# Kernel optimization log

Measured on AMD Instinct MI355X. Metric: run time of the kernel, lower is better.

## Reference

```python
import jax, jax.numpy as jnp
import numpy as np

N_NODES = 50000
IN_CH = 256
HID_CH = 64
N_EDGES = 800000


def setup_inputs() -> dict:
    key = jax.random.key(0)
    k1, k2, k3, k4, k5 = jax.random.split(key, 5)
    x = jax.random.normal(k1, (N_NODES, IN_CH), dtype=jnp.float32)
    edge_index = jax.random.randint(k2, (2, N_EDGES), 0, N_NODES, dtype=jnp.int64)
    # GCNConv linear weight (Glorot) and zero bias, as in PyG defaults
    W = jax.random.normal(k3, (IN_CH, HID_CH), dtype=jnp.float32) * (1.0 / np.sqrt(IN_CH))
    bias = jnp.zeros((HID_CH,), dtype=jnp.float32)
    # PReLU per-channel weight, torch default init 0.25
    prelu_a = jnp.full((HID_CH,), 0.25, dtype=jnp.float32)
    return {"x": x, "edge_index": edge_index, "W": W, "bias": bias, "prelu_a": prelu_a}


def reference(x, edge_index, W, bias, prelu_a):
    # GCNConv, normalize=False: transform then scatter-add over edges, + bias
    xw = x @ W                               # [N, H]
    src, dst = edge_index[0], edge_index[1]
    msgs = xw[src]                           # [E, H] gather
    agg = jax.ops.segment_sum(msgs, dst, num_segments=N_NODES)  # [N, H]
    out = agg + bias
    # per-channel PReLU
    return jnp.where(out > 0, out, prelu_a * out)
```

## Files before the change

kernel.cpp:

```cpp
#include <hip/hip_runtime.h>

#define N_NODES 50000
#define IN_CH   256
#define HID_CH  64
#define N_EDGES 800000

#define NBUCKET 391
#define AG_ROWS 128
#define PTILE   4096
#define CAP     4096

typedef __attribute__((ext_vector_type(8))) short short8;
typedef __attribute__((ext_vector_type(4))) float f32x4;

static __device__ __forceinline__ unsigned short f2bf(float f) {
    unsigned int u = __float_as_uint(f);
    u += 0x7FFF + ((u >> 16) & 1);
    return (unsigned short)(u >> 16);
}
static __device__ __forceinline__ float bf2f(unsigned short h) {
    return __uint_as_float(((unsigned int)h) << 16);
}

__global__ __launch_bounds__(256) void wfrag_kernel(const float* __restrict__ W,
                                                    unsigned short* __restrict__ wfrag) {
    const int idx = blockIdx.x * 256 + threadIdx.x;
    if (idx >= 2048) return;
    const int ks = idx >> 8;
    const int nt = (idx >> 6) & 3;
    const int l  = idx & 63;
    const int q = l >> 4, m = l & 15;
    const int n = nt * 16 + m;
    const int k0 = ks * 32 + q * 8;
    short8 v;
    #pragma unroll
    for (int j = 0; j < 8; ++j) v[j] = (short)f2bf(W[(k0 + j) * HID_CH + n]);
    ((short8*)wfrag)[idx] = v;
}

__global__ __launch_bounds__(256) void gemm_kernel(const float* __restrict__ x,
                                                   const unsigned short* __restrict__ wfrag,
                                                   unsigned short* __restrict__ xwb) {
    const int wave = threadIdx.x >> 6;
    const int lane = threadIdx.x & 63;
    const int q = lane >> 4, m = lane & 15;
    const int row0 = blockIdx.x * 64 + wave * 16;
    const int arow = row0 + m;
    const int arl = arow < N_NODES ? arow : N_NODES - 1;
    const float* xr = x + (size_t)arl * IN_CH + q * 8;
    const short8* wf = (const short8*)wfrag;

    f32x4 acc0 = {0.f,0.f,0.f,0.f}, acc1 = acc0, acc2 = acc0, acc3 = acc0;

    #pragma unroll
    for (int ks = 0; ks < 8; ++ks) {
        const float4 a0 = *(const float4*)(xr + ks * 32);
        const float4 a1 = *(const float4*)(xr + ks * 32 + 4);
        short8 af;
        af[0] = (short)f2bf(a0.x); af[1] = (short)f2bf(a0.y);
        af[2] = (short)f2bf(a0.z); af[3] = (short)f2bf(a0.w);
        af[4] = (short)f2bf(a1.x); af[5] = (short)f2bf(a1.y);
        af[6] = (short)f2bf(a1.z); af[7] = (short)f2bf(a1.w);
        const short8 b0 = wf[(ks * 4 + 0) * 64 + lane];
        const short8 b1 = wf[(ks * 4 + 1) * 64 + lane];
        const short8 b2 = wf[(ks * 4 + 2) * 64 + lane];
        const short8 b3 = wf[(ks * 4 + 3) * 64 + lane];
        acc0 = __builtin_amdgcn_mfma_f32_16x16x32_bf16(af, b0, acc0, 0, 0, 0);
        acc1 = __builtin_amdgcn_mfma_f32_16x16x32_bf16(af, b1, acc1, 0, 0, 0);
        acc2 = __builtin_amdgcn_mfma_f32_16x16x32_bf16(af, b2, acc2, 0, 0, 0);
        acc3 = __builtin_amdgcn_mfma_f32_16x16x32_bf16(af, b3, acc3, 0, 0, 0);
    }

    #pragma unroll
    for (int r = 0; r < 4; ++r) {
        const int row = row0 + q * 4 + r;
        if (row < N_NODES) {
            unsigned short* o = xwb + (size_t)row * HID_CH + m;
            o[0]  = f2bf(acc0[r]);
            o[16] = f2bf(acc1[r]);
            o[32] = f2bf(acc2[r]);
            o[48] = f2bf(acc3[r]);
        }
    }
}

__global__ __launch_bounds__(256) void bhist_kernel(const int* __restrict__ ei,
                                                    int* __restrict__ cnt) {
    __shared__ int h[NBUCKET];
    for (int i = threadIdx.x; i < NBUCKET; i += 256) h[i] = 0;
    __syncthreads();
    for (int e = blockIdx.x * 256 + threadIdx.x; e < N_EDGES; e += gridDim.x * 256)
        atomicAdd(&h[ei[N_EDGES + e] >> 7], 1);
    __syncthreads();
    for (int i = threadIdx.x; i < NBUCKET; i += 256)
        if (h[i]) atomicAdd(&cnt[i], h[i]);
}

__global__ __launch_bounds__(512) void bscan_kernel(int* __restrict__ cur,
                                                    int* __restrict__ bucket_off) {
    __shared__ int s[512];
    const int t = threadIdx.x;
    const int v = (t < NBUCKET) ? cur[t] : 0;
    s[t] = v;
    __syncthreads();
    for (int off = 1; off < 512; off <<= 1) {
        const int a = s[t];
        const int add = (t >= off) ? s[t - off] : 0;
        __syncthreads();
        s[t] = a + add;
        __syncthreads();
    }
    const int ex = s[t] - v;
    if (t < NBUCKET) { bucket_off[t] = ex; cur[t] = ex; }
    if (t == 0) bucket_off[NBUCKET] = N_EDGES;
}

__global__ __launch_bounds__(512) void partition_kernel(const int* __restrict__ ei,
                                                        int* __restrict__ cur,
                                                        unsigned int* __restrict__ packed_out) {
    __shared__ int cnt[512];
    __shared__ int excl[512];
    __shared__ int lcur[512];
    __shared__ int gbase[512];
    __shared__ unsigned int staged[PTILE];
    __shared__ unsigned short sbkt[PTILE];

    const int t = threadIdx.x;
    const int tile0 = blockIdx.x * PTILE;
    const int tcnt = min(PTILE, N_EDGES - tile0);

    cnt[t] = 0;
    __syncthreads();

    int es[8], ed[8];
    #pragma unroll
    for (int i = 0; i < 8; ++i) {
        const int e = tile0 + t + i * 512;
        if (e < N_EDGES) {
            es[i] = ei[e];
            ed[i] = ei[N_EDGES + e];
            atomicAdd(&cnt[ed[i] >> 7], 1);
        } else es[i] = -1;
    }
    __syncthreads();

    const int v = cnt[t];
    excl[t] = v;
    __syncthreads();
    for (int off = 1; off < 512; off <<= 1) {
        const int a = excl[t];
        const int add = (t >= off) ? excl[t - off] : 0;
        __syncthreads();
        excl[t] = a + add;
        __syncthreads();
    }
    const int ex = excl[t] - v;
    __syncthreads();
    excl[t] = ex;
    lcur[t] = ex;
    if (t < NBUCKET && v > 0) gbase[t] = atomicAdd(&cur[t], v);
    __syncthreads();

    #pragma unroll
    for (int i = 0; i < 8; ++i) {
        if (es[i] >= 0) {
            const int b = ed[i] >> 7;
            const int pos = atomicAdd(&lcur[b], 1);
            staged[pos] = ((unsigned int)(ed[i] & 127) << 16) | (unsigned int)es[i];
            sbkt[pos] = (unsigned short)b;
        }
    }
    __syncthreads();

    #pragma unroll
    for (int i = 0; i < 8; ++i) {
        const int idx = t + i * 512;
        if (idx < tcnt) {
            const int b = sbkt[idx];
            packed_out[gbase[b] + (idx - excl[b])] = staged[idx];
        }
    }
}

__global__ __launch_bounds__(1024) void aggregate_kernel(const unsigned short* __restrict__ xwb,
                                                         const unsigned int* __restrict__ packed,
                                                         const int* __restrict__ bucket_off,
                                                         const float* __restrict__ bias,
                                                         const float* __restrict__ prelu_a,
                                                         float* __restrict__ out) {
    __shared__ unsigned int   sp[CAP];
    __shared__ unsigned short ssrc[CAP];
    __shared__ int hcnt[AG_ROWS];
    __shared__ int hexcl[AG_ROWS];
    __shared__ int hcur[AG_ROWS];
    __shared__ float acc[AG_ROWS * HID_CH];

    const int b = blockIdx.x;
    const int t = threadIdx.x;
    const int beg = bucket_off[b], end = bucket_off[b + 1];
    const int wv = t >> 6, lane = t & 63;
    const int slot = lane >> 4, c0 = (lane & 15) * 4;

    #pragma unroll
    for (int i = 0; i < 8; ++i) acc[t + i * 1024] = 0.f;

    for (int cbeg = beg; cbeg < end; cbeg += CAP) {
        const int csz = min(CAP, end - cbeg);

        if (t < AG_ROWS) hcnt[t] = 0;
        __syncthreads();

        for (int i = t; i < csz; i += 1024) {
            const unsigned int p = packed[cbeg + i];
            sp[i] = p;
            atomicAdd(&hcnt[p >> 16], 1);
        }
        __syncthreads();

        if (t < AG_ROWS) hexcl[t] = hcnt[t];
        __syncthreads();
        for (int off = 1; off < AG_ROWS; off <<= 1) {
            int nv = 0;
            if (t < AG_ROWS) { nv = hexcl[t]; if (t >= off) nv += hexcl[t - off]; }
            __syncthreads();
            if (t < AG_ROWS) hexcl[t] = nv;
            __syncthreads();
        }
        if (t < AG_ROWS) { const int e = hexcl[t] - hcnt[t]; hexcl[t] = e; hcur[t] = e; }
        __syncthreads();

        for (int i = t; i < csz; i += 1024) {
            const unsigned int p = sp[i];
            const int pos = atomicAdd(&hcur[p >> 16], 1);
            ssrc[pos] = (unsigned short)(p & 0xFFFFu);
        }
        __syncthreads();

        #pragma unroll
        for (int k = 0; k < 8; ++k) {
            const int nl = wv + k * 16;
            const int rb = hexcl[nl];
            const int re = rb + hcnt[nl];
            float4 a4 = make_float4(0.f, 0.f, 0.f, 0.f);
            for (int i = rb + slot; i < re; i += 4) {
                const int s = ssrc[i];
                const ushort4 v = *(const ushort4*)(xwb + (size_t)s * HID_CH + c0);
                a4.x += bf2f(v.x); a4.y += bf2f(v.y);
                a4.z += bf2f(v.z); a4.w += bf2f(v.w);
            }
            a4.x += __shfl_xor(a4.x, 16, 64); a4.y += __shfl_xor(a4.y, 16, 64);
            a4.z += __shfl_xor(a4.z, 16, 64); a4.w += __shfl_xor(a4.w, 16, 64);
            a4.x += __shfl_xor(a4.x, 32, 64); a4.y += __shfl_xor(a4.y, 32, 64);
            a4.z += __shfl_xor(a4.z, 32, 64); a4.w += __shfl_xor(a4.w, 32, 64);
            if (slot == 0) {
                float4* ap = (float4*)&acc[nl * HID_CH + c0];
                float4 c4 = *ap;
                c4.x += a4.x; c4.y += a4.y; c4.z += a4.z; c4.w += a4.w;
                *ap = c4;
            }
        }
        __syncthreads();
    }

    const int node0 = b * AG_ROWS;
    const int nrows = min(AG_ROWS, N_NODES - node0);
    for (int i = t; i < nrows * (HID_CH / 4); i += 1024) {
        const int r = i >> 4;
        const int cc = (i & 15) * 4;
        const float4 a4 = *(float4*)&acc[r * HID_CH + cc];
        const float4 bb = *(const float4*)(bias + cc);
        const float4 aa = *(const float4*)(prelu_a + cc);
        float4 rr;
        rr.x = a4.x + bb.x; rr.x = rr.x > 0.f ? rr.x : aa.x * rr.x;
        rr.y = a4.y + bb.y; rr.y = rr.y > 0.f ? rr.y : aa.y * rr.y;
        rr.z = a4.z + bb.z; rr.z = rr.z > 0.f ? rr.z : aa.z * rr.z;
        rr.w = a4.w + bb.w; rr.w = rr.w > 0.f ? rr.w : aa.w * rr.w;
        *(float4*)(out + (size_t)(node0 + r) * HID_CH + cc) = rr;
    }
}

extern "C" void kernel_launch(void* const* d_in, const int* in_sizes, int n_in,
                              void* d_out, int out_size, void* d_ws, size_t ws_size,
                              hipStream_t stream) {
    const float* x       = (const float*)d_in[0];
    const int*   ei      = (const int*)d_in[1];
    const float* W       = (const float*)d_in[2];
    const float* bias    = (const float*)d_in[3];
    const float* prelu_a = (const float*)d_in[4];
    float* out = (float*)d_out;

    char* w = (char*)d_ws;
    unsigned short* xwb        = (unsigned short*)(w);
    int*            cur        = (int*)(w + 6400000);
    int*            bucket_off = (int*)(w + 6401600);
    unsigned int*   packed     = (unsigned int*)(w + 6403200);
    unsigned short* wfrag      = (unsigned short*)(w + 9603200);

    wfrag_kernel<<<8, 256, 0, stream>>>(W, wfrag);

    gemm_kernel<<<(N_NODES + 63) / 64, 256, 0, stream>>>(x, wfrag, xwb);

    hipMemsetAsync(cur, 0, NBUCKET * sizeof(int), stream);
    bhist_kernel<<<256, 256, 0, stream>>>(ei, cur);

    bscan_kernel<<<1, 512, 0, stream>>>(cur, bucket_off);

    partition_kernel<<<(N_EDGES + PTILE - 1) / PTILE, 512, 0, stream>>>(ei, cur, packed);

    aggregate_kernel<<<NBUCKET, 1024, 0, stream>>>(xwb, packed, bucket_off, bias, prelu_a, out);
}
```

Measured before the change: 152.3 us.

## Use fixed-capacity edge buckets to drop histogram and scan kernels

```diff
diff --git a/kernel.cpp b/kernel.cpp
--- a/kernel.cpp
+++ b/kernel.cpp
@@ -5,10 +5,11 @@
 #define HID_CH  64
 #define N_EDGES 800000
 
-#define NBUCKET 391
-#define AG_ROWS 128
+#define AG_ROWS 64
+#define NBUCKET 782
+#define CAPB    1536
 #define PTILE   4096
-#define CAP     4096
+#define CAP     2048
 
 typedef __attribute__((ext_vector_type(8))) short short8;
 typedef __attribute__((ext_vector_type(4))) float f32x4;
@@ -84,44 +85,13 @@
     }
 }
 
-__global__ __launch_bounds__(256) void bhist_kernel(const int* __restrict__ ei,
-                                                    int* __restrict__ cnt) {
-    __shared__ int h[NBUCKET];
-    for (int i = threadIdx.x; i < NBUCKET; i += 256) h[i] = 0;
-    __syncthreads();
-    for (int e = blockIdx.x * 256 + threadIdx.x; e < N_EDGES; e += gridDim.x * 256)
-        atomicAdd(&h[ei[N_EDGES + e] >> 7], 1);
-    __syncthreads();
-    for (int i = threadIdx.x; i < NBUCKET; i += 256)
-        if (h[i]) atomicAdd(&cnt[i], h[i]);
-}
-
-__global__ __launch_bounds__(512) void bscan_kernel(int* __restrict__ cur,
-                                                    int* __restrict__ bucket_off) {
-    __shared__ int s[512];
-    const int t = threadIdx.x;
-    const int v = (t < NBUCKET) ? cur[t] : 0;
-    s[t] = v;
-    __syncthreads();
-    for (int off = 1; off < 512; off <<= 1) {
-        const int a = s[t];
-        const int add = (t >= off) ? s[t - off] : 0;
-        __syncthreads();
-        s[t] = a + add;
-        __syncthreads();
-    }
-    const int ex = s[t] - v;
-    if (t < NBUCKET) { bucket_off[t] = ex; cur[t] = ex; }
-    if (t == 0) bucket_off[NBUCKET] = N_EDGES;
-}
-
-__global__ __launch_bounds__(512) void partition_kernel(const int* __restrict__ ei,
-                                                        int* __restrict__ cur,
-                                                        unsigned int* __restrict__ packed_out) {
-    __shared__ int cnt[512];
-    __shared__ int excl[512];
-    __shared__ int lcur[512];
-    __shared__ int gbase[512];
+__global__ __launch_bounds__(1024) void partition_kernel(const int* __restrict__ ei,
+                                                         int* __restrict__ cnt,
+                                                         unsigned int* __restrict__ packed_out) {
+    __shared__ int hcnt[1024];
+    __shared__ int excl[1024];
+    __shared__ int lcur[1024];
+    __shared__ int gbase[1024];
     __shared__ unsigned int staged[PTILE];
     __shared__ unsigned short sbkt[PTILE];
 
@@ -129,25 +99,25 @@
     const int tile0 = blockIdx.x * PTILE;
     const int tcnt = min(PTILE, N_EDGES - tile0);
 
-    cnt[t] = 0;
-    __syncthreads();
-
-    int es[8], ed[8];
-    #pragma unroll
-    for (int i = 0; i < 8; ++i) {
-        const int e = tile0 + t + i * 512;
+    hcnt[t] = 0;
+    __syncthreads();
+
+    int es[4], ed[4];
+    #pragma unroll
+    for (int i = 0; i < 4; ++i) {
+        const int e = tile0 + t + i * 1024;
         if (e < N_EDGES) {
             es[i] = ei[e];
             ed[i] = ei[N_EDGES + e];
-            atomicAdd(&cnt[ed[i] >> 7], 1);
+            atomicAdd(&hcnt[ed[i] >> 6], 1);
         } else es[i] = -1;
     }
     __syncthreads();
 
-    const int v = cnt[t];
+    const int v = hcnt[t];
     excl[t] = v;
     __syncthreads();
-    for (int off = 1; off < 512; off <<= 1) {
+    for (int off = 1; off < 1024; off <<= 1) {
         const int a = excl[t];
         const int add = (t >= off) ? excl[t - off] : 0;
         __syncthreads();
@@ -158,23 +128,23 @@
     __syncthreads();
     excl[t] = ex;
     lcur[t] = ex;
-    if (t < NBUCKET && v > 0) gbase[t] = atomicAdd(&cur[t], v);
-    __syncthreads();
-
-    #pragma unroll
-    for (int i = 0; i < 8; ++i) {
+    if (t < NBUCKET && v > 0) gbase[t] = t * CAPB + atomicAdd(&cnt[t], v);
+    __syncthreads();
+
+    #pragma unroll
+    for (int i = 0; i < 4; ++i) {
         if (es[i] >= 0) {
-            const int b = ed[i] >> 7;
+            const int b = ed[i] >> 6;
             const int pos = atomicAdd(&lcur[b], 1);
-            staged[pos] = ((unsigned int)(ed[i] & 127) << 16) | (unsigned int)es[i];
+            staged[pos] = ((unsigned int)(ed[i] & 63) << 16) | (unsigned int)es[i];
             sbkt[pos] = (unsigned short)b;
         }
     }
     __syncthreads();
 
     #pragma unroll
-    for (int i = 0; i < 8; ++i) {
-        const int idx = t + i * 512;
+    for (int i = 0; i < 4; ++i) {
+        const int idx = t + i * 1024;
         if (idx < tcnt) {
             const int b = sbkt[idx];
             packed_out[gbase[b] + (idx - excl[b])] = staged[idx];
@@ -182,12 +152,12 @@
     }
 }
 
-__global__ __launch_bounds__(1024) void aggregate_kernel(const unsigned short* __restrict__ xwb,
-                                                         const unsigned int* __restrict__ packed,
-                                                         const int* __restrict__ bucket_off,
-                                                         const float* __restrict__ bias,
-                                                         const float* __restrict__ prelu_a,
-                                                         float* __restrict__ out) {
+__global__ __launch_bounds__(512) void aggregate_kernel(const unsigned short* __restrict__ xwb,
+                                                        const unsigned int* __restrict__ packed,
+                                                        const int* __restrict__ cnt,
+                                                        const float* __restrict__ bias,
+                                                        const float* __restrict__ prelu_a,
+                                                        float* __restrict__ out) {
     __shared__ unsigned int   sp[CAP];
     __shared__ unsigned short ssrc[CAP];
     __shared__ int hcnt[AG_ROWS];
@@ -197,21 +167,22 @@
 
     const int b = blockIdx.x;
     const int t = threadIdx.x;
-    const int beg = bucket_off[b], end = bucket_off[b + 1];
+    const int beg = b * CAPB;
+    const int total = cnt[b];
     const int wv = t >> 6, lane = t & 63;
     const int slot = lane >> 4, c0 = (lane & 15) * 4;
 
     #pragma unroll
-    for (int i = 0; i < 8; ++i) acc[t + i * 1024] = 0.f;
-
-    for (int cbeg = beg; cbeg < end; cbeg += CAP) {
-        const int csz = min(CAP, end - cbeg);
+    for (int i = 0; i < 8; ++i) acc[t + i * 512] = 0.f;
+
+    for (int cbeg = 0; cbeg < total; cbeg += CAP) {
+        const int csz = min(CAP, total - cbeg);
 
         if (t < AG_ROWS) hcnt[t] = 0;
         __syncthreads();
 
-        for (int i = t; i < csz; i += 1024) {
-            const unsigned int p = packed[cbeg + i];
+        for (int i = t; i < csz; i += 512) {
+            const unsigned int p = packed[beg + cbeg + i];
             sp[i] = p;
             atomicAdd(&hcnt[p >> 16], 1);
         }
@@ -229,7 +200,7 @@
         if (t < AG_ROWS) { const int e = hexcl[t] - hcnt[t]; hexcl[t] = e; hcur[t] = e; }
         __syncthreads();
 
-        for (int i = t; i < csz; i += 1024) {
+        for (int i = t; i < csz; i += 512) {
             const unsigned int p = sp[i];
             const int pos = atomicAdd(&hcur[p >> 16], 1);
             ssrc[pos] = (unsigned short)(p & 0xFFFFu);
@@ -238,16 +209,29 @@
 
         #pragma unroll
         for (int k = 0; k < 8; ++k) {
-            const int nl = wv + k * 16;
+            const int nl = wv * 8 + k;
             const int rb = hexcl[nl];
             const int re = rb + hcnt[nl];
             float4 a4 = make_float4(0.f, 0.f, 0.f, 0.f);
-            for (int i = rb + slot; i < re; i += 4) {
+            float4 b4 = make_float4(0.f, 0.f, 0.f, 0.f);
+            int i = rb + slot;
+            for (; i + 4 < re; i += 8) {
+                const int s0 = ssrc[i];
+                const int s1 = ssrc[i + 4];
+                const ushort4 v0 = *(const ushort4*)(xwb + (size_t)s0 * HID_CH + c0);
+                const ushort4 v1 = *(const ushort4*)(xwb + (size_t)s1 * HID_CH + c0);
+                a4.x += bf2f(v0.x); a4.y += bf2f(v0.y);
+                a4.z += bf2f(v0.z); a4.w += bf2f(v0.w);
+                b4.x += bf2f(v1.x); b4.y += bf2f(v1.y);
+                b4.z += bf2f(v1.z); b4.w += bf2f(v1.w);
+            }
+            if (i < re) {
                 const int s = ssrc[i];
                 const ushort4 v = *(const ushort4*)(xwb + (size_t)s * HID_CH + c0);
                 a4.x += bf2f(v.x); a4.y += bf2f(v.y);
                 a4.z += bf2f(v.z); a4.w += bf2f(v.w);
             }
+            a4.x += b4.x; a4.y += b4.y; a4.z += b4.z; a4.w += b4.w;
             a4.x += __shfl_xor(a4.x, 16, 64); a4.y += __shfl_xor(a4.y, 16, 64);
             a4.z += __shfl_xor(a4.z, 16, 64); a4.w += __shfl_xor(a4.w, 16, 64);
             a4.x += __shfl_xor(a4.x, 32, 64); a4.y += __shfl_xor(a4.y, 32, 64);
@@ -264,7 +248,7 @@
 
     const int node0 = b * AG_ROWS;
     const int nrows = min(AG_ROWS, N_NODES - node0);
-    for (int i = t; i < nrows * (HID_CH / 4); i += 1024) {
+    for (int i = t; i < nrows * (HID_CH / 4); i += 512) {
         const int r = i >> 4;
         const int cc = (i & 15) * 4;
         const float4 a4 = *(float4*)&acc[r * HID_CH + cc];
@@ -290,22 +274,18 @@
     float* out = (float*)d_out;
 
     char* w = (char*)d_ws;
-    unsigned short* xwb        = (unsigned short*)(w);
-    int*            cur        = (int*)(w + 6400000);
-    int*            bucket_off = (int*)(w + 6401600);
-    unsigned int*   packed     = (unsigned int*)(w + 6403200);
-    unsigned short* wfrag      = (unsigned short*)(w + 9603200);
+    unsigned short* xwb    = (unsigned short*)(w);
+    int*            cnt    = (int*)(w + 6400000);
+    unsigned int*   packed = (unsigned int*)(w + 6403200);
+    unsigned short* wfrag  = (unsigned short*)(w + 11207808);
 
     wfrag_kernel<<<8, 256, 0, stream>>>(W, wfrag);
 
     gemm_kernel<<<(N_NODES + 63) / 64, 256, 0, stream>>>(x, wfrag, xwb);
 
-    hipMemsetAsync(cur, 0, NBUCKET * sizeof(int), stream);
-    bhist_kernel<<<256, 256, 0, stream>>>(ei, cur);
-
-    bscan_kernel<<<1, 512, 0, stream>>>(cur, bucket_off);
-
-    partition_kernel<<<(N_EDGES + PTILE - 1) / PTILE, 512, 0, stream>>>(ei, cur, packed);
-
-    aggregate_kernel<<<NBUCKET, 1024, 0, stream>>>(xwb, packed, bucket_off, bias, prelu_a, out);
-}
+    hipMemsetAsync(cnt, 0, NBUCKET * sizeof(int), stream);
+
+    partition_kernel<<<(N_EDGES + PTILE - 1) / PTILE, 1024, 0, stream>>>(ei, cnt, packed);
+
+    aggregate_kernel<<<NBUCKET, 512, 0, stream>>>(xwb, packed, cnt, bias, prelu_a, out);
+}
```

Result: faster. 135.9 us (-10.8%).
